# Kernel tuning notes

Hardware: AMD Instinct MI355X
Metric: run time of the kernel (lower is better)

Reference implementation:

```python
import jax, jax.numpy as jnp
import numpy as np

EPS = 1e-06
LN_EPS = 1e-05
N_OP, N_MAC = 50000, 2000
IN_OP, IN_MAC, OUT, HEADS = 64, 32, 128, 4
DK = OUT // HEADS
ATT_DIM = 2 * DK + 1
E_SEQ, E_OM, E_MO = 150000, 300000, 300000


def setup_inputs() -> dict:
    key = jax.random.key(0)
    ks = jax.random.split(key, 20)
    return {
        "h_op": jax.random.normal(ks[0], (N_OP, IN_OP), jnp.float32),
        "h_mac": jax.random.normal(ks[1], (N_MAC, IN_MAC), jnp.float32),
        "seq_src": jax.random.randint(ks[2], (E_SEQ,), 0, N_OP),
        "seq_dst": jax.random.randint(ks[3], (E_SEQ,), 0, N_OP),
        "op_mac_src": jax.random.randint(ks[4], (E_OM,), 0, N_OP),
        "op_mac_dst": jax.random.randint(ks[5], (E_OM,), 0, N_MAC),
        "mac_op_src": jax.random.randint(ks[6], (E_MO,), 0, N_MAC),
        "mac_op_dst": jax.random.randint(ks[7], (E_MO,), 0, N_OP),
        "feat_seq": jax.random.normal(ks[8], (E_SEQ, 1), jnp.float32),
        "feat_op_mac": jax.random.normal(ks[9], (E_OM, 1), jnp.float32),
        "feat_mac_op": jax.random.normal(ks[10], (E_MO, 1), jnp.float32),
        "W_op_w": jax.random.normal(ks[11], (OUT, IN_OP), jnp.float32) / np.sqrt(IN_OP),
        "W_op_b": jnp.zeros((OUT,), jnp.float32),
        "W_mac_w": jax.random.normal(ks[12], (OUT, IN_MAC), jnp.float32) / np.sqrt(IN_MAC),
        "W_mac_b": jnp.zeros((OUT,), jnp.float32),
        "att_seq": jax.random.normal(ks[13], (HEADS, ATT_DIM), jnp.float32),
        "att_op_mac": jax.random.normal(ks[14], (HEADS, ATT_DIM), jnp.float32),
        "att_mac_op": jax.random.normal(ks[15], (HEADS, ATT_DIM), jnp.float32),
        "ln_op_g": jnp.ones((OUT,), jnp.float32),
        "ln_op_b": jnp.zeros((OUT,), jnp.float32),
        "ln_mac_g": jnp.ones((OUT,), jnp.float32),
        "ln_mac_b": jnp.zeros((OUT,), jnp.float32),
    }


def _apply_attn(src_emb, dst_emb, src_idx, dst_idx, feat_e, att, n_dst):
    # src_emb: [Ns,H,Dk], dst_emb: [Nd,H,Dk], feat_e: [E,1], att: [H,2*Dk+1]
    h_s = src_emb[src_idx]                                  # [E,H,Dk] gather
    h_d = dst_emb[dst_idx]                                  # [E,H,Dk] gather
    f_e = jnp.broadcast_to(feat_e[:, None, :], (feat_e.shape[0], HEADS, 1))
    concat = jnp.concatenate([h_s, h_d, f_e], axis=-1)      # [E,H,2*Dk+1]
    scores = jnp.sum(concat * att, axis=-1)                 # [E,H]
    scores = jnp.clip(jax.nn.leaky_relu(scores, 0.2), -20.0, 20.0)
    alpha = jnp.exp(scores)                                 # [E,H]
    denom = jax.ops.segment_sum(alpha, dst_idx, num_segments=n_dst)[dst_idx] + EPS
    weighted = h_s * (alpha / denom)[..., None]             # [E,H,Dk]
    return jax.ops.segment_sum(weighted, dst_idx, num_segments=n_dst)  # [Nd,H,Dk]


def _layernorm(x, g, b):
    mu = jnp.mean(x, axis=-1, keepdims=True)
    var = jnp.mean(jnp.square(x - mu), axis=-1, keepdims=True)
    return (x - mu) * jax.lax.rsqrt(var + LN_EPS) * g + b


def reference(h_op, h_mac, seq_src, seq_dst, op_mac_src, op_mac_dst,
              mac_op_src, mac_op_dst, feat_seq, feat_op_mac, feat_mac_op,
              W_op_w, W_op_b, W_mac_w, W_mac_b,
              att_seq, att_op_mac, att_mac_op,
              ln_op_g, ln_op_b, ln_mac_g, ln_mac_b):
    z_op_flat = h_op @ W_op_w.T + W_op_b                    # [N_op, OUT]
    z_mac_flat = h_mac @ W_mac_w.T + W_mac_b                # [N_mac, OUT]
    z_op = z_op_flat.reshape(-1, HEADS, DK)
    z_mac = z_mac_flat.reshape(-1, HEADS, DK)

    out_op = _apply_attn(z_op, z_op, seq_src, seq_dst, feat_seq, att_seq, z_op.shape[0])
    out_op = out_op + _apply_attn(z_mac, z_op, mac_op_src, mac_op_dst, feat_mac_op, att_mac_op, z_op.shape[0])
    out_mac = _apply_attn(z_op, z_mac, op_mac_src, op_mac_dst, feat_op_mac, att_op_mac, z_mac.shape[0])

    res_op = out_op.reshape(-1, OUT) + z_op_flat
    res_mac = out_mac.reshape(-1, OUT) + z_mac_flat
    res_op = _layernorm(res_op, ln_op_g, ln_op_b)
    res_mac = _layernorm(res_mac, ln_mac_g, ln_mac_b)
    return jax.nn.elu(res_op), jax.nn.elu(res_mac)
```

## Files before the change

### kernel.cpp

```cpp
#include <hip/hip_runtime.h>

#define N_OP   50000
#define N_MAC  2000
#define IN_OP  64
#define IN_MAC 32
#define OUT    128
#define HEADS  4
#define DK     32
#define ATT_DIM 65
#define E_SEQ  150000
#define E_OM   300000
#define E_MO   300000
#define TOT_E  (E_SEQ + E_MO + E_OM)
#define EPS    1e-6f
#define LN_EPS 1e-5f
#define NXCD   8

#define TILES_OP  (N_OP / 16)
#define TILES_MAC (N_MAC / 16)
#define GBA ((TILES_OP + 3) / 4)
#define GBB ((TILES_MAC + 3) / 4)
#define HBK ((TOT_E + 511) / 512)

#define AB_OP   ((N_OP + 255) / 256)
#define AB_OM   ((N_MAC + 255) / 256)
#define AB_TOT  (AB_OP + AB_OM)

#define FALL_B  ((TOT_E + 255) / 256)
#define GOP_B   ((N_OP + 3) / 4)

typedef unsigned short ushort_t;
typedef unsigned int   uint_t;
typedef __attribute__((ext_vector_type(8))) short bf16x8;
typedef __attribute__((ext_vector_type(4))) float f32x4;

__device__ __forceinline__ ushort_t f32_to_bf16_rtne(float f) {
    uint_t u = __float_as_uint(f);
    u += 0x7FFFu + ((u >> 16) & 1u);
    return (ushort_t)(u >> 16);
}

__device__ __forceinline__ bf16x8 cvt8(float4 a, float4 b) {
    bf16x8 r;
    r[0] = (short)f32_to_bf16_rtne(a.x); r[1] = (short)f32_to_bf16_rtne(a.y);
    r[2] = (short)f32_to_bf16_rtne(a.z); r[3] = (short)f32_to_bf16_rtne(a.w);
    r[4] = (short)f32_to_bf16_rtne(b.x); r[5] = (short)f32_to_bf16_rtne(b.y);
    r[6] = (short)f32_to_bf16_rtne(b.z); r[7] = (short)f32_to_bf16_rtne(b.w);
    return r;
}

__device__ __forceinline__ uint_t my_xcd() {
    uint_t x;
    asm volatile("s_getreg_b32 %0, hwreg(HW_REG_XCC_ID)" : "=s"(x));
    return x & (NXCD - 1);
}

__device__ __forceinline__ int l2_atomic_inc(int* p) {
    return __hip_atomic_fetch_add(p, 1, __ATOMIC_RELAXED, __HIP_MEMORY_SCOPE_WORKGROUP);
}

__global__ void k_fold_zero(const float* __restrict__ W_op, const float* __restrict__ b_op,
                            const float* __restrict__ W_mac, const float* __restrict__ b_mac,
                            const float* __restrict__ att_seq, const float* __restrict__ att_om,
                            const float* __restrict__ att_mo,
                            float* __restrict__ c_op, float* __restrict__ c_mac,
                            ushort_t* __restrict__ Ub_op, ushort_t* __restrict__ Ub_mac,
                            int* __restrict__ zero_base) {
    const int t = threadIdx.x;
    if (blockIdx.x == 0) {
        for (int idx = t; idx < 16 * IN_OP; idx += 256) {
            const int j = idx >> 6, k = idx & 63;
            const int hd = j & 3, pr = j >> 2;
            const float* att = (pr <= 1) ? att_seq : (pr == 2 ? att_om : att_mo);
            const int off = (pr == 1 || pr == 3) ? 32 : 0;
            float s = 0.f;
            for (int l = 0; l < 32; ++l)
                s += att[hd * ATT_DIM + off + l] * W_op[(hd * 32 + l) * IN_OP + k];
            Ub_op[idx] = f32_to_bf16_rtne(s);
        }
        if (t < 16) {
            const int hd = t & 3, pr = t >> 2;
            const float* att = (pr <= 1) ? att_seq : (pr == 2 ? att_om : att_mo);
            const int off = (pr == 1 || pr == 3) ? 32 : 0;
            float s = 0.f;
            for (int l = 0; l < 32; ++l) s += att[hd * ATT_DIM + off + l] * b_op[hd * 32 + l];
            c_op[t] = s;
        }
        for (int idx = t; idx < 8 * IN_MAC; idx += 256) {
            const int j = idx >> 5, k = idx & 31;
            const int hd = j & 3, pr = j >> 2;
            const float* att = (pr == 0) ? att_om : att_mo;
            const int off = (pr == 0) ? 32 : 0;
            float s = 0.f;
            for (int l = 0; l < 32; ++l)
                s += att[hd * ATT_DIM + off + l] * W_mac[(hd * 32 + l) * IN_MAC + k];
            Ub_mac[idx] = f32_to_bf16_rtne(s);
        }
        for (int idx = 8 * IN_MAC + t; idx < 16 * IN_MAC; idx += 256) Ub_mac[idx] = 0;
        if (t < 8) {
            const int hd = t & 3, pr = t >> 2;
            const float* att = (pr == 0) ? att_om : att_mo;
            const int off = (pr == 0) ? 32 : 0;
            float s = 0.f;
            for (int l = 0; l < 32; ++l) s += att[hd * ATT_DIM + off + l] * b_mac[hd * 32 + l];
            c_mac[t] = s;
        }
    } else {
        const int n = NXCD * (N_OP + N_MAC) + 4;
        for (int i = (blockIdx.x - 1) * 256 + t; i < n; i += 63 * 256)
            zero_base[i] = 0;
    }
}

__global__ void k_gemm_histo(
    const float* __restrict__ h_op, const float* __restrict__ W_op, const float* __restrict__ b_op,
    const float* __restrict__ h_mac, const float* __restrict__ W_mac, const float* __restrict__ b_mac,
    const ushort_t* __restrict__ Ub_op, const float* __restrict__ c_op,
    const ushort_t* __restrict__ Ub_mac, const float* __restrict__ c_mac,
    ushort_t* __restrict__ zb_op, ushort_t* __restrict__ zb_mac,
    float* __restrict__ p_op, float* __restrict__ p_mac,
    const int* __restrict__ seq_dst, const int* __restrict__ mo_dst, const int* __restrict__ om_dst,
    int* __restrict__ crep_op, int* __restrict__ crep_om,
    int* __restrict__ rank_all) {
    const int bid = blockIdx.x;
    const int t = threadIdx.x;
    const int w = t >> 6, l = t & 63;
    const int li = l & 15, lg = l >> 4;

    if (bid < GBA) {
        const int tile = bid * 4 + w;
        if (tile >= TILES_OP) return;
        const int row0 = tile * 16;
        const float* hr = h_op + (size_t)(row0 + li) * IN_OP + lg * 8;
        const bf16x8 a0 = cvt8(*reinterpret_cast<const float4*>(hr),
                               *reinterpret_cast<const float4*>(hr + 4));
        const bf16x8 a1 = cvt8(*reinterpret_cast<const float4*>(hr + 32),
                               *reinterpret_cast<const float4*>(hr + 36));
        const int orow = row0 + lg * 4;
#pragma unroll
        for (int ct = 0; ct < 8; ++ct) {
            const int col = ct * 16 + li;
            const float* wr = W_op + (size_t)col * IN_OP + lg * 8;
            const bf16x8 b0 = cvt8(*reinterpret_cast<const float4*>(wr),
                                   *reinterpret_cast<const float4*>(wr + 4));
            const bf16x8 b1 = cvt8(*reinterpret_cast<const float4*>(wr + 32),
                                   *reinterpret_cast<const float4*>(wr + 36));
            f32x4 acc = {0.f, 0.f, 0.f, 0.f};
            acc = __builtin_amdgcn_mfma_f32_16x16x32_bf16(a0, b0, acc, 0, 0, 0);
            acc = __builtin_amdgcn_mfma_f32_16x16x32_bf16(a1, b1, acc, 0, 0, 0);
            const float bias = b_op[col];
#pragma unroll
            for (int r = 0; r < 4; ++r)
                zb_op[(size_t)(orow + r) * OUT + col] = f32_to_bf16_rtne(acc[r] + bias);
        }
        {
            const bf16x8 u0 = *reinterpret_cast<const bf16x8*>(Ub_op + (size_t)li * IN_OP + lg * 8);
            const bf16x8 u1 = *reinterpret_cast<const bf16x8*>(Ub_op + (size_t)li * IN_OP + lg * 8 + 32);
            f32x4 acc = {0.f, 0.f, 0.f, 0.f};
            acc = __builtin_amdgcn_mfma_f32_16x16x32_bf16(a0, u0, acc, 0, 0, 0);
            acc = __builtin_amdgcn_mfma_f32_16x16x32_bf16(a1, u1, acc, 0, 0, 0);
            const float cj = c_op[li];
#pragma unroll
            for (int r = 0; r < 4; ++r)
                p_op[(size_t)(orow + r) * 16 + li] = acc[r] + cj;
        }
    } else if (bid < GBA + GBB) {
        const int tile = (bid - GBA) * 4 + w;
        if (tile >= TILES_MAC) return;
        const int row0 = tile * 16;
        const float* hr = h_mac + (size_t)(row0 + li) * IN_MAC + lg * 8;
        const bf16x8 a0 = cvt8(*reinterpret_cast<const float4*>(hr),
                               *reinterpret_cast<const float4*>(hr + 4));
        const int orow = row0 + lg * 4;
#pragma unroll
        for (int ct = 0; ct < 8; ++ct) {
            const int col = ct * 16 + li;
            const float* wr = W_mac + (size_t)col * IN_MAC + lg * 8;
            const bf16x8 b0 = cvt8(*reinterpret_cast<const float4*>(wr),
                                   *reinterpret_cast<const float4*>(wr + 4));
            f32x4 acc = {0.f, 0.f, 0.f, 0.f};
            acc = __builtin_amdgcn_mfma_f32_16x16x32_bf16(a0, b0, acc, 0, 0, 0);
            const float bias = b_mac[col];
#pragma unroll
            for (int r = 0; r < 4; ++r)
                zb_mac[(size_t)(orow + r) * OUT + col] = f32_to_bf16_rtne(acc[r] + bias);
        }
        {
            const bf16x8 u0 = *reinterpret_cast<const bf16x8*>(Ub_mac + (size_t)li * IN_MAC + lg * 8);
            f32x4 acc = {0.f, 0.f, 0.f, 0.f};
            acc = __builtin_amdgcn_mfma_f32_16x16x32_bf16(a0, u0, acc, 0, 0, 0);
            if (li < 8) {
                const float cj = c_mac[li];
#pragma unroll
                for (int r = 0; r < 4; ++r)
                    p_mac[(size_t)(orow + r) * 8 + li] = acc[r] + cj;
            }
        }
    } else {
        const uint_t x = my_xcd();
        int* const cop = crep_op + x * N_OP;
        int* const com = crep_om + x * N_MAC;
        const int base = (bid - GBA - GBB) * 512 + t;
#pragma unroll
        for (int k = 0; k < 2; ++k) {
            const int ge = base + k * 256;
            int r;
            if (ge < E_SEQ) {
                r = l2_atomic_inc(&cop[seq_dst[ge]]);
                rank_all[ge] = (int)((x << 24) | (uint_t)r);
            } else if (ge < E_SEQ + E_MO) {
                r = l2_atomic_inc(&cop[mo_dst[ge - E_SEQ]]);
                rank_all[ge] = (int)((x << 24) | (uint_t)r);
            } else if (ge < TOT_E) {
                r = l2_atomic_inc(&com[om_dst[ge - E_SEQ - E_MO]]);
                rank_all[ge] = (int)((x << 24) | (uint_t)r);
            }
        }
    }
}

__global__ void k_alloc(const int* __restrict__ crep_op, int* __restrict__ sta_op, int* __restrict__ end_op, int* __restrict__ brep_op,
                        const int* __restrict__ crep_om, int* __restrict__ sta_om, int* __restrict__ end_om, int* __restrict__ brep_om,
                        int* __restrict__ ctr) {
    const int b = blockIdx.x, t = threadIdx.x;
    const int* crep; int* sta; int* end; int* brep; int n, g, lb;
    if (b < AB_OP) { crep = crep_op; sta = sta_op; end = end_op; brep = brep_op; n = N_OP;  g = 0; lb = b; }
    else           { crep = crep_om; sta = sta_om; end = end_om; brep = brep_om; n = N_MAC; g = 1; lb = b - AB_OP; }
    const int d = lb * 256 + t;
    const int lane = t & 63;
    int c[NXCD];
    int tot = 0;
#pragma unroll
    for (int x = 0; x < NXCD; ++x) {
        c[x] = (d < n) ? crep[x * n + d] : 0;
        tot += c[x];
    }
    int xs = tot;
#pragma unroll
    for (int m = 1; m < 64; m <<= 1) {
        int y = __shfl_up(xs, m);
        if (lane >= m) xs += y;
    }
    int base = 0;
    if (lane == 63) base = atomicAdd(&ctr[g], xs);
    base = __shfl(base, 63);
    if (d < n) {
        const int s = base + xs - tot;
        sta[d] = s;
        end[d] = s + tot;
        int acc = s;
#pragma unroll
        for (int x = 0; x < NXCD; ++x) {
            brep[x * n + d] = acc;
            acc += c[x];
        }
    }
}

__device__ __forceinline__ void fill_one(uint_t rowtag, int d, float f,
                                         const float* __restrict__ ps, int pso,
                                         const float* __restrict__ pd, int pdo,
                                         const float* __restrict__ att,
                                         const int* __restrict__ brep, int n, int ri,
                                         uint4* __restrict__ rec) {
    const float4 as = *reinterpret_cast<const float4*>(ps + pso);
    const float4 ad = *reinterpret_cast<const float4*>(pd + pdo);
    const float4 aw = make_float4(att[64], att[ATT_DIM + 64], att[2 * ATT_DIM + 64], att[3 * ATT_DIM + 64]);
    const float sc[4] = {as.x + ad.x + f * aw.x, as.y + ad.y + f * aw.y,
                         as.z + ad.z + f * aw.z, as.w + ad.w + f * aw.w};
    uint_t b16[4];
#pragma unroll
    for (int hh = 0; hh < 4; ++hh) {
        float v = sc[hh];
        v = (v >= 0.f) ? v : 0.2f * v;
        v = fminf(fmaxf(v, -20.f), 20.f);
        b16[hh] = f32_to_bf16_rtne(expf(v));
    }
    const int xcd = ((uint_t)ri) >> 24;
    const int rank = ri & 0xFFFFFF;
    const int pos = brep[xcd * n + d] + rank;
    uint4 r;
    r.x = rowtag;
    r.y = b16[0] | (b16[1] << 16);
    r.z = b16[2] | (b16[3] << 16);
    r.w = 0;
    rec[pos] = r;
}

__global__ void k_fill(
    const int* __restrict__ seq_src, const int* __restrict__ seq_dst, const float* __restrict__ feat_seq,
    const int* __restrict__ mo_src,  const int* __restrict__ mo_dst,  const float* __restrict__ feat_mo,
    const int* __restrict__ om_src,  const int* __restrict__ om_dst,  const float* __restrict__ feat_om,
    const float* __restrict__ p_op, const float* __restrict__ p_mac,
    const float* __restrict__ att_seq, const float* __restrict__ att_mo, const float* __restrict__ att_om,
    const int* __restrict__ brep_op, const int* __restrict__ brep_om,
    const int* __restrict__ rank_all,
    uint4* __restrict__ rec_op, uint4* __restrict__ rec_om) {
    const int ge = blockIdx.x * 256 + threadIdx.x;
    if (ge < E_SEQ) {
        const int s = seq_src[ge], d = seq_dst[ge];
        fill_one((uint_t)s, d, feat_seq[ge], p_op, s * 16 + 0, p_op, d * 16 + 4,
                 att_seq, brep_op, N_OP, rank_all[ge], rec_op);
    } else if (ge < E_SEQ + E_MO) {
        const int e = ge - E_SEQ;
        const int s = mo_src[e], d = mo_dst[e];
        fill_one((uint_t)(N_OP + s) | 0x80000000u, d, feat_mo[e], p_mac, s * 8 + 4,
                 p_op, d * 16 + 12, att_mo, brep_op, N_OP, rank_all[ge], rec_op);
    } else if (ge < TOT_E) {
        const int e = ge - E_SEQ - E_MO;
        const int s = om_src[e], d = om_dst[e];
        fill_one((uint_t)s, d, feat_om[e], p_op, s * 16 + 8, p_mac, d * 8 + 0,
                 att_om, brep_om, N_MAC, rank_all[ge], rec_om);
    }
}

__device__ __forceinline__ float2 ln_elu2(float x0, float x1, int lane,
                                          const float* __restrict__ g,
                                          const float* __restrict__ bb, int col2) {
    float s = x0 + x1;
#pragma unroll
    for (int m = 32; m >= 1; m >>= 1) s += __shfl_xor(s, m);
    const float mu = s * (1.0f / OUT);
    const float dx0 = x0 - mu, dx1 = x1 - mu;
    float q = dx0 * dx0 + dx1 * dx1;
#pragma unroll
    for (int m = 32; m >= 1; m >>= 1) q += __shfl_xor(q, m);
    const float r = rsqrtf(q * (1.0f / OUT) + LN_EPS);
    const float2 g2 = *reinterpret_cast<const float2*>(g + col2);
    const float2 b2 = *reinterpret_cast<const float2*>(bb + col2);
    float y0 = dx0 * r * g2.x + b2.x;
    float y1 = dx1 * r * g2.y + b2.y;
    y0 = (y0 > 0.f) ? y0 : expm1f(y0);
    y1 = (y1 > 0.f) ? y1 : expm1f(y1);
    return make_float2(y0, y1);
}

__device__ __forceinline__ float2 unpack_bf2(uint_t zz) {
    return make_float2(__uint_as_float(zz << 16), __uint_as_float(zz & 0xffff0000u));
}

__device__ __forceinline__ void seg_scalar(const uint4* __restrict__ rec,
                                           const ushort_t* __restrict__ arena,
                                           int s0, int e0, int wSel, int hiSel, int col2,
                                           float& ns0, float& ns1, float& nm0, float& nm1,
                                           float& ds, float& dm) {
#pragma unroll 8
    for (int i = s0; i < e0; ++i) {
        const uint4 r = rec[i];
        const int row = (int)(r.x & 0x7fffffffu);
        const uint_t isMo = r.x >> 31;
        const uint_t pick = wSel ? r.z : r.y;
        const float a = __uint_as_float(hiSel ? (pick & 0xffff0000u) : (pick << 16));
        const float a_s = isMo ? 0.f : a;
        const float a_m = isMo ? a : 0.f;
        const uint_t zz = *reinterpret_cast<const uint_t*>(arena + (size_t)row * OUT + col2);
        const float z0 = __uint_as_float(zz << 16);
        const float z1 = __uint_as_float(zz & 0xffff0000u);
        ns0 = fmaf(a_s, z0, ns0);
        ns1 = fmaf(a_s, z1, ns1);
        nm0 = fmaf(a_m, z0, nm0);
        nm1 = fmaf(a_m, z1, nm1);
        ds += a_s;
        dm += a_m;
    }
}

__global__ void k_gather(
    const uint4* __restrict__ rec_op, const int* __restrict__ sta_op, const int* __restrict__ end_op,
    const uint4* __restrict__ rec_om, const int* __restrict__ sta_om, const int* __restrict__ end_om,
    const ushort_t* __restrict__ zb_op, const ushort_t* __restrict__ zb_mac,
    const float* __restrict__ g_op, const float* __restrict__ b_op,
    const float* __restrict__ g_mac, const float* __restrict__ b_mac,
    float* __restrict__ out_op, float* __restrict__ out_mac) {
    const int bid = blockIdx.x;
    const int t = threadIdx.x;
    const int w = __builtin_amdgcn_readfirstlane(t >> 6);
    const int lane = t & 63;
    const int hd = lane >> 4;
    const int col2 = lane * 2;
    const int wSel = hd >> 1, hiSel = hd & 1;
    __shared__ float nsh[4][OUT];
    __shared__ float dsh[4][2 * HEADS];

    if (bid < GOP_B) {
        const int d = __builtin_amdgcn_readfirstlane(bid * 4 + w);
        if (d >= N_OP) return;
        const int s0 = sta_op[d], e0 = end_op[d];
        float ns0 = 0.f, ns1 = 0.f, nm0 = 0.f, nm1 = 0.f, ds = 0.f, dm = 0.f;
        seg_scalar(rec_op, zb_op, s0, e0, wSel, hiSel, col2, ns0, ns1, nm0, nm1, ds, dm);
        const float invS = 1.0f / (ds + EPS);
        const float invM = 1.0f / (dm + EPS);
        const float acc0 = ns0 * invS + nm0 * invM;
        const float acc1 = ns1 * invS + nm1 * invM;
        const float2 zr = unpack_bf2(*reinterpret_cast<const uint_t*>(zb_op + (size_t)d * OUT + col2));
        const float2 o2 = ln_elu2(acc0 + zr.x, acc1 + zr.y, lane, g_op, b_op, col2);
        *reinterpret_cast<float2*>(out_op + (size_t)d * OUT + col2) = o2;
    } else {
        const int d = __builtin_amdgcn_readfirstlane(bid - GOP_B);
        const int s0 = sta_om[d], e0 = end_om[d];
        const int len = e0 - s0;
        const int quarter = (len + 3) >> 2;
        const int i0 = s0 + w * quarter;
        int i1 = i0 + quarter;
        if (i1 > e0) i1 = e0;
        float ns0 = 0.f, ns1 = 0.f, nm0 = 0.f, nm1 = 0.f, ds = 0.f, dm = 0.f;
        if (i0 < e0)
            seg_scalar(rec_om, zb_op, i0, i1, wSel, hiSel, col2, ns0, ns1, nm0, nm1, ds, dm);
        nsh[w][col2] = ns0;
        nsh[w][col2 + 1] = ns1;
        if ((lane & 15) == 0) dsh[w][hd] = ds;
        __syncthreads();
        if (w == 0) {
            const float n0 = nsh[0][col2] + nsh[1][col2] + nsh[2][col2] + nsh[3][col2];
            const float n1 = nsh[0][col2 + 1] + nsh[1][col2 + 1] + nsh[2][col2 + 1] + nsh[3][col2 + 1];
            const float dt = dsh[0][hd] + dsh[1][hd] + dsh[2][hd] + dsh[3][hd];
            const float inv = 1.0f / (dt + EPS);
            const float2 zr = unpack_bf2(*reinterpret_cast<const uint_t*>(zb_mac + (size_t)d * OUT + col2));
            const float2 o2 = ln_elu2(n0 * inv + zr.x, n1 * inv + zr.y, lane, g_mac, b_mac, col2);
            *reinterpret_cast<float2*>(out_mac + (size_t)d * OUT + col2) = o2;
        }
    }
}

extern "C" void kernel_launch(void* const* d_in, const int* in_sizes, int n_in,
                              void* d_out, int out_size, void* d_ws, size_t ws_size,
                              hipStream_t stream) {
    const float* h_op      = (const float*)d_in[0];
    const float* h_mac     = (const float*)d_in[1];
    const int*   seq_src   = (const int*)d_in[2];
    const int*   seq_dst   = (const int*)d_in[3];
    const int*   om_src    = (const int*)d_in[4];
    const int*   om_dst    = (const int*)d_in[5];
    const int*   mo_src    = (const int*)d_in[6];
    const int*   mo_dst    = (const int*)d_in[7];
    const float* feat_seq  = (const float*)d_in[8];
    const float* feat_om   = (const float*)d_in[9];
    const float* feat_mo   = (const float*)d_in[10];
    const float* W_op_w    = (const float*)d_in[11];
    const float* W_op_b    = (const float*)d_in[12];
    const float* W_mac_w   = (const float*)d_in[13];
    const float* W_mac_b   = (const float*)d_in[14];
    const float* att_seq   = (const float*)d_in[15];
    const float* att_om    = (const float*)d_in[16];
    const float* att_mo    = (const float*)d_in[17];
    const float* ln_op_g   = (const float*)d_in[18];
    const float* ln_op_b   = (const float*)d_in[19];
    const float* ln_mac_g  = (const float*)d_in[20];
    const float* ln_mac_b  = (const float*)d_in[21];

    float* p = (float*)d_ws;
    float* p_op   = p; p += (size_t)N_OP * 16;
    float* p_mac  = p; p += (size_t)N_MAC * 8;
    float* c_op   = p; p += 16;
    float* c_mac  = p; p += 16;
    uint4* rec_op = (uint4*)p; p += (size_t)(E_SEQ + E_MO) * 4;
    uint4* rec_om = (uint4*)p; p += (size_t)E_OM * 4;
    ushort_t* zb_op  = (ushort_t*)p; p += (size_t)N_OP * OUT / 2;
    ushort_t* zb_mac = (ushort_t*)p; p += (size_t)N_MAC * OUT / 2;
    ushort_t* Ub_op  = (ushort_t*)p; p += 16 * IN_OP / 2;
    ushort_t* Ub_mac = (ushort_t*)p; p += 16 * IN_MAC / 2;
    int* q = (int*)p;
    int* crep_op = q; q += NXCD * N_OP;
    int* crep_om = q; q += NXCD * N_MAC;
    int* ctr     = q; q += 4;
    int* sta_op = q; q += N_OP;
    int* sta_om = q; q += N_MAC;
    int* end_op = q; q += N_OP;
    int* end_om = q; q += N_MAC;
    int* brep_op = q; q += NXCD * N_OP;
    int* brep_om = q; q += NXCD * N_MAC;
    int* rank_all = q; q += TOT_E;

    float* out_op  = (float*)d_out;
    float* out_mac = (float*)d_out + (size_t)N_OP * OUT;

    k_fold_zero<<<64, 256, 0, stream>>>(W_op_w, W_op_b, W_mac_w, W_mac_b,
                                        att_seq, att_om, att_mo,
                                        c_op, c_mac, Ub_op, Ub_mac, crep_op);

    k_gemm_histo<<<GBA + GBB + HBK, 256, 0, stream>>>(
        h_op, W_op_w, W_op_b, h_mac, W_mac_w, W_mac_b,
        Ub_op, c_op, Ub_mac, c_mac,
        zb_op, zb_mac, p_op, p_mac,
        seq_dst, mo_dst, om_dst, crep_op, crep_om, rank_all);

    k_alloc<<<AB_TOT, 256, 0, stream>>>(
        crep_op, sta_op, end_op, brep_op,
        crep_om, sta_om, end_om, brep_om, ctr);

    k_fill<<<FALL_B, 256, 0, stream>>>(
        seq_src, seq_dst, feat_seq, mo_src, mo_dst, feat_mo, om_src, om_dst, feat_om,
        p_op, p_mac, att_seq, att_mo, att_om,
        brep_op, brep_om, rank_all,
        rec_op, rec_om);

    k_gather<<<GOP_B + N_MAC, 256, 0, stream>>>(
        rec_op, sta_op, end_op,
        rec_om, sta_om, end_om,
        zb_op, zb_mac,
        ln_op_g, ln_op_b, ln_mac_g, ln_mac_b,
        out_op, out_mac);
}
```

Baseline: 124.5 us.

## Overlap op-edge record fill with mac-node gather by re-splitting kernels

The single fill kernel is split in two. The op->mac edge fill runs first, and the seq/mac->op edge fill is fused into the same launch as the mac-node gather, so the two independent pieces of work share one grid. The op-node gather then moves to its own kernel. Fill threads now handle two edges each. This adds one launch and changes the block mix, so load balance between the long mac gather blocks and the fill blocks may be uneven.

```diff
diff --git a/kernel.cpp b/kernel.cpp
--- a/kernel.cpp
+++ b/kernel.cpp
@@ -11,6 +11,7 @@
 #define E_SEQ  150000
 #define E_OM   300000
 #define E_MO   300000
+#define E_SM   (E_SEQ + E_MO)
 #define TOT_E  (E_SEQ + E_MO + E_OM)
 #define EPS    1e-6f
 #define LN_EPS 1e-5f
@@ -26,7 +27,8 @@
 #define AB_OM   ((N_MAC + 255) / 256)
 #define AB_TOT  (AB_OP + AB_OM)
 
-#define FALL_B  ((TOT_E + 255) / 256)
+#define FOM_B   ((E_OM + 511) / 512)
+#define FSM_B   ((E_SM + 511) / 512)
 #define GOP_B   ((N_OP + 3) / 4)
 
 typedef unsigned short ushort_t;
@@ -208,11 +210,11 @@
             if (ge < E_SEQ) {
                 r = l2_atomic_inc(&cop[seq_dst[ge]]);
                 rank_all[ge] = (int)((x << 24) | (uint_t)r);
-            } else if (ge < E_SEQ + E_MO) {
+            } else if (ge < E_SM) {
                 r = l2_atomic_inc(&cop[mo_dst[ge - E_SEQ]]);
                 rank_all[ge] = (int)((x << 24) | (uint_t)r);
             } else if (ge < TOT_E) {
-                r = l2_atomic_inc(&com[om_dst[ge - E_SEQ - E_MO]]);
+                r = l2_atomic_inc(&com[om_dst[ge - E_SM]]);
                 rank_all[ge] = (int)((x << 24) | (uint_t)r);
             }
         }
@@ -287,30 +289,41 @@
     rec[pos] = r;
 }
 
-__global__ void k_fill(
+__device__ __forceinline__ void fill_sm_edge(
+    int ge,
     const int* __restrict__ seq_src, const int* __restrict__ seq_dst, const float* __restrict__ feat_seq,
     const int* __restrict__ mo_src,  const int* __restrict__ mo_dst,  const float* __restrict__ feat_mo,
-    const int* __restrict__ om_src,  const int* __restrict__ om_dst,  const float* __restrict__ feat_om,
     const float* __restrict__ p_op, const float* __restrict__ p_mac,
-    const float* __restrict__ att_seq, const float* __restrict__ att_mo, const float* __restrict__ att_om,
-    const int* __restrict__ brep_op, const int* __restrict__ brep_om,
-    const int* __restrict__ rank_all,
-    uint4* __restrict__ rec_op, uint4* __restrict__ rec_om) {
-    const int ge = blockIdx.x * 256 + threadIdx.x;
+    const float* __restrict__ att_seq, const float* __restrict__ att_mo,
+    const int* __restrict__ brep_op, const int* __restrict__ rank_all,
+    uint4* __restrict__ rec_op) {
     if (ge < E_SEQ) {
         const int s = seq_src[ge], d = seq_dst[ge];
         fill_one((uint_t)s, d, feat_seq[ge], p_op, s * 16 + 0, p_op, d * 16 + 4,
                  att_seq, brep_op, N_OP, rank_all[ge], rec_op);
-    } else if (ge < E_SEQ + E_MO) {
+    } else if (ge < E_SM) {
         const int e = ge - E_SEQ;
         const int s = mo_src[e], d = mo_dst[e];
         fill_one((uint_t)(N_OP + s) | 0x80000000u, d, feat_mo[e], p_mac, s * 8 + 4,
                  p_op, d * 16 + 12, att_mo, brep_op, N_OP, rank_all[ge], rec_op);
-    } else if (ge < TOT_E) {
-        const int e = ge - E_SEQ - E_MO;
-        const int s = om_src[e], d = om_dst[e];
-        fill_one((uint_t)s, d, feat_om[e], p_op, s * 16 + 8, p_mac, d * 8 + 0,
-                 att_om, brep_om, N_MAC, rank_all[ge], rec_om);
+    }
+}
+
+__global__ void k_fill_om(
+    const int* __restrict__ om_src, const int* __restrict__ om_dst, const float* __restrict__ feat_om,
+    const float* __restrict__ p_op, const float* __restrict__ p_mac,
+    const float* __restrict__ att_om,
+    const int* __restrict__ brep_om, const int* __restrict__ rank_all,
+    uint4* __restrict__ rec_om) {
+    const int base = blockIdx.x * 512 + threadIdx.x;
+#pragma unroll
+    for (int k = 0; k < 2; ++k) {
+        const int e = base + k * 256;
+        if (e < E_OM) {
+            const int s = om_src[e], d = om_dst[e];
+            fill_one((uint_t)s, d, feat_om[e], p_op, s * 16 + 8, p_mac, d * 8 + 0,
+                     att_om, brep_om, N_MAC, rank_all[E_SM + e], rec_om);
+        }
     }
 }
 
@@ -365,38 +378,28 @@
     }
 }
 
-__global__ void k_gather(
-    const uint4* __restrict__ rec_op, const int* __restrict__ sta_op, const int* __restrict__ end_op,
+__global__ void k_gmac_fillsm(
     const uint4* __restrict__ rec_om, const int* __restrict__ sta_om, const int* __restrict__ end_om,
     const ushort_t* __restrict__ zb_op, const ushort_t* __restrict__ zb_mac,
-    const float* __restrict__ g_op, const float* __restrict__ b_op,
     const float* __restrict__ g_mac, const float* __restrict__ b_mac,
-    float* __restrict__ out_op, float* __restrict__ out_mac) {
+    float* __restrict__ out_mac,
+    const int* __restrict__ seq_src, const int* __restrict__ seq_dst, const float* __restrict__ feat_seq,
+    const int* __restrict__ mo_src,  const int* __restrict__ mo_dst,  const float* __restrict__ feat_mo,
+    const float* __restrict__ p_op, const float* __restrict__ p_mac,
+    const float* __restrict__ att_seq, const float* __restrict__ att_mo,
+    const int* __restrict__ brep_op, const int* __restrict__ rank_all,
+    uint4* __restrict__ rec_op) {
     const int bid = blockIdx.x;
     const int t = threadIdx.x;
-    const int w = __builtin_amdgcn_readfirstlane(t >> 6);
-    const int lane = t & 63;
-    const int hd = lane >> 4;
-    const int col2 = lane * 2;
-    const int wSel = hd >> 1, hiSel = hd & 1;
-    __shared__ float nsh[4][OUT];
-    __shared__ float dsh[4][2 * HEADS];
-
-    if (bid < GOP_B) {
-        const int d = __builtin_amdgcn_readfirstlane(bid * 4 + w);
-        if (d >= N_OP) return;
-        const int s0 = sta_op[d], e0 = end_op[d];
-        float ns0 = 0.f, ns1 = 0.f, nm0 = 0.f, nm1 = 0.f, ds = 0.f, dm = 0.f;
-        seg_scalar(rec_op, zb_op, s0, e0, wSel, hiSel, col2, ns0, ns1, nm0, nm1, ds, dm);
-        const float invS = 1.0f / (ds + EPS);
-        const float invM = 1.0f / (dm + EPS);
-        const float acc0 = ns0 * invS + nm0 * invM;
-        const float acc1 = ns1 * invS + nm1 * invM;
-        const float2 zr = unpack_bf2(*reinterpret_cast<const uint_t*>(zb_op + (size_t)d * OUT + col2));
-        const float2 o2 = ln_elu2(acc0 + zr.x, acc1 + zr.y, lane, g_op, b_op, col2);
-        *reinterpret_cast<float2*>(out_op + (size_t)d * OUT + col2) = o2;
-    } else {
-        const int d = __builtin_amdgcn_readfirstlane(bid - GOP_B);
+    if (bid < N_MAC) {
+        const int w = __builtin_amdgcn_readfirstlane(t >> 6);
+        const int lane = t & 63;
+        const int hd = lane >> 4;
+        const int col2 = lane * 2;
+        const int wSel = hd >> 1, hiSel = hd & 1;
+        __shared__ float nsh[4][OUT];
+        __shared__ float dsh[4][2 * HEADS];
+        const int d = __builtin_amdgcn_readfirstlane(bid);
         const int s0 = sta_om[d], e0 = end_om[d];
         const int len = e0 - s0;
         const int quarter = (len + 3) >> 2;
@@ -419,7 +422,39 @@
             const float2 o2 = ln_elu2(n0 * inv + zr.x, n1 * inv + zr.y, lane, g_mac, b_mac, col2);
             *reinterpret_cast<float2*>(out_mac + (size_t)d * OUT + col2) = o2;
         }
-    }
+    } else {
+        const int base = (bid - N_MAC) * 512 + t;
+#pragma unroll
+        for (int k = 0; k < 2; ++k) {
+            fill_sm_edge(base + k * 256, seq_src, seq_dst, feat_seq, mo_src, mo_dst, feat_mo,
+                         p_op, p_mac, att_seq, att_mo, brep_op, rank_all, rec_op);
+        }
+    }
+}
+
+__global__ void k_gather_op(
+    const uint4* __restrict__ rec_op, const int* __restrict__ sta_op, const int* __restrict__ end_op,
+    const ushort_t* __restrict__ zb_op,
+    const float* __restrict__ g_op, const float* __restrict__ b_op,
+    float* __restrict__ out_op) {
+    const int t = threadIdx.x;
+    const int w = __builtin_amdgcn_readfirstlane(t >> 6);
+    const int lane = t & 63;
+    const int hd = lane >> 4;
+    const int col2 = lane * 2;
+    const int wSel = hd >> 1, hiSel = hd & 1;
+    const int d = __builtin_amdgcn_readfirstlane(blockIdx.x * 4 + w);
+    if (d >= N_OP) return;
+    const int s0 = sta_op[d], e0 = end_op[d];
+    float ns0 = 0.f, ns1 = 0.f, nm0 = 0.f, nm1 = 0.f, ds = 0.f, dm = 0.f;
+    seg_scalar(rec_op, zb_op, s0, e0, wSel, hiSel, col2, ns0, ns1, nm0, nm1, ds, dm);
+    const float invS = 1.0f / (ds + EPS);
+    const float invM = 1.0f / (dm + EPS);
+    const float acc0 = ns0 * invS + nm0 * invM;
+    const float acc1 = ns1 * invS + nm1 * invM;
+    const float2 zr = unpack_bf2(*reinterpret_cast<const uint_t*>(zb_op + (size_t)d * OUT + col2));
+    const float2 o2 = ln_elu2(acc0 + zr.x, acc1 + zr.y, lane, g_op, b_op, col2);
+    *reinterpret_cast<float2*>(out_op + (size_t)d * OUT + col2) = o2;
 }
 
 extern "C" void kernel_launch(void* const* d_in, const int* in_sizes, int n_in,
@@ -453,7 +488,7 @@
     float* p_mac  = p; p += (size_t)N_MAC * 8;
     float* c_op   = p; p += 16;
     float* c_mac  = p; p += 16;
-    uint4* rec_op = (uint4*)p; p += (size_t)(E_SEQ + E_MO) * 4;
+    uint4* rec_op = (uint4*)p; p += (size_t)E_SM * 4;
     uint4* rec_om = (uint4*)p; p += (size_t)E_OM * 4;
     ushort_t* zb_op  = (ushort_t*)p; p += (size_t)N_OP * OUT / 2;
     ushort_t* zb_mac = (ushort_t*)p; p += (size_t)N_MAC * OUT / 2;
@@ -488,16 +523,15 @@
         crep_op, sta_op, end_op, brep_op,
         crep_om, sta_om, end_om, brep_om, ctr);
 
-    k_fill<<<FALL_B, 256, 0, stream>>>(
-        seq_src, seq_dst, feat_seq, mo_src, mo_dst, feat_mo, om_src, om_dst, feat_om,
-        p_op, p_mac, att_seq, att_mo, att_om,
-        brep_op, brep_om, rank_all,
-        rec_op, rec_om);
-
-    k_gather<<<GOP_B + N_MAC, 256, 0, stream>>>(
-        rec_op, sta_op, end_op,
-        rec_om, sta_om, end_om,
-        zb_op, zb_mac,
-        ln_op_g, ln_op_b, ln_mac_g, ln_mac_b,
-        out_op, out_mac);
-}
+    k_fill_om<<<FOM_B, 256, 0, stream>>>(
+        om_src, om_dst, feat_om, p_op, p_mac, att_om,
+        brep_om, rank_all, rec_om);
+
+    k_gmac_fillsm<<<N_MAC + FSM_B, 256, 0, stream>>>(
+        rec_om, sta_om, end_om, zb_op, zb_mac, ln_mac_g, ln_mac_b, out_mac,
+        seq_src, seq_dst, feat_seq, mo_src, mo_dst, feat_mo,
+        p_op, p_mac, att_seq, att_mo, brep_op, rank_all, rec_op);
+
+    k_gather_op<<<GOP_B, 256, 0, stream>>>(
+        rec_op, sta_op, end_op, zb_op, ln_op_g, ln_op_b, out_op);
+}
```

After: 135.7 us. +9.0%, slower.
